# Kernel optimization log

Hardware: AMD Instinct MI355X
Metric: run time of the kernel (lower is better)

The kernel has to match this reference:

```python
import jax, jax.numpy as jnp
import numpy as np

N_LAYERS = 2
H = 16                      # num_heads
ARW = (1.0, 1.0)            # att_residual_weight
MCB = (0.0, 1.0)            # mask_clip_balancer
LN_EPS = 1e-5


def _ln(x, g, b):
    mu = jnp.mean(x, axis=-1, keepdims=True)
    var = jnp.mean(jnp.square(x - mu), axis=-1, keepdims=True)
    return (x - mu) * jax.lax.rsqrt(var + LN_EPS) * g + b


def _quick_gelu(u):
    return u * jax.nn.sigmoid(1.702 * u)


def setup_inputs() -> dict:
    key = jax.random.key(0)
    ks = jax.random.split(key, 8)
    L, B, C = 577, 8, 1024
    d_ff = 4 * C
    inp = {
        'x': jax.random.normal(ks[0], (L, B, C), jnp.float32),
        'att_bias': jax.random.normal(ks[1], (N_LAYERS, B * H, L, L), jnp.float32),
        'ln1_g': jnp.ones((N_LAYERS, C), jnp.float32),
        'ln1_b': jnp.zeros((N_LAYERS, C), jnp.float32),
        'in_w': 0.02 * jax.random.normal(ks[2], (N_LAYERS, 3 * C, C), jnp.float32),
        'in_b': jnp.zeros((N_LAYERS, 3 * C), jnp.float32),
        'out_w': 0.02 * jax.random.normal(ks[3], (N_LAYERS, C, C), jnp.float32),
        'out_b': jnp.zeros((N_LAYERS, C), jnp.float32),
        'ln2_g': jnp.ones((N_LAYERS, C), jnp.float32),
        'ln2_b': jnp.zeros((N_LAYERS, C), jnp.float32),
        'fc1_w': 0.02 * jax.random.normal(ks[4], (N_LAYERS, d_ff, C), jnp.float32),
        'fc1_b': jnp.zeros((N_LAYERS, d_ff), jnp.float32),
        'fc2_w': 0.02 * jax.random.normal(ks[5], (N_LAYERS, C, d_ff), jnp.float32),
        'fc2_b': jnp.zeros((N_LAYERS, C), jnp.float32),
    }
    return inp


def reference(x, att_bias, ln1_g, ln1_b, in_w, in_b, out_w, out_b,
              ln2_g, ln2_b, fc1_w, fc1_b, fc2_w, fc2_b):
    L, B, C = x.shape
    d = C // H
    scale = d ** -0.5  # custom_att_factor is None
    for i in range(N_LAYERS):
        # --- custom CSA attention ---
        h = _ln(x, ln1_g[i], ln1_b[i])                              # [L,B,C]
        qkv = jnp.einsum('lbc,fc->lbf', h, in_w[i]) + in_b[i]       # [L,B,3C]
        q, k, v = jnp.split(qkv, 3, axis=-1)
        to_heads = lambda t: t.reshape(L, B, H, d).transpose(1, 2, 0, 3)  # [B,H,L,d]
        q, k, v = to_heads(q), to_heads(k), to_heads(v)
        bias = att_bias[i].reshape(B, H, L, L)
        q_attn = bias + scale * jnp.einsum('bhld,bhmd->bhlm', q, q)
        k_attn = bias + scale * jnp.einsum('bhld,bhmd->bhlm', k, k)
        attn = jax.nn.softmax(q_attn, axis=-1) + jax.nn.softmax(k_attn, axis=-1)
        attn = attn * 0.5                                           # norm_att=True
        attn = jnp.mean(attn, axis=1, keepdims=True)                # avg_att=True -> [B,1,L,L]
        out = jnp.matmul(attn, v)                                   # broadcast over H -> [B,H,L,d]
        out = MCB[0] * v + MCB[1] * out
        out = out.transpose(2, 0, 1, 3).reshape(L, B, C)
        out = jnp.einsum('lbc,oc->lbo', out, out_w[i]) + out_b[i]
        x = ARW[0] * x + ARW[1] * out
        # --- MLP residual ---
        h2 = _ln(x, ln2_g[i], ln2_b[i])
        u = _quick_gelu(jnp.einsum('lbc,fc->lbf', h2, fc1_w[i]) + fc1_b[i])
        x = x + jnp.einsum('lbf,cf->lbc', u, fc2_w[i]) + fc2_b[i]
    return x
```

## Files before the change

kernel.cpp:

```cpp
#include <hip/hip_runtime.h>

typedef float f32x4 __attribute__((ext_vector_type(4)));
typedef __bf16 bf16x8 __attribute__((ext_vector_type(8)));

#define L_SEQ 577
#define BB 8
#define CC 1024
#define HH 16
#define ROWS (L_SEQ*BB)

static __device__ __forceinline__ ushort f2b(float f) {
  unsigned u = __float_as_uint(f);
  u += 0x7fffu + ((u >> 16) & 1u);
  return (ushort)(u >> 16);
}

static __device__ __forceinline__ void gld16(const void* g, void* l) {
  __builtin_amdgcn_global_load_lds((const __attribute__((address_space(1))) void*)g,
                                   (__attribute__((address_space(3))) void*)l, 16, 0, 0);
}

__global__ void cvt4_kernel(const float* __restrict__ s0, ushort* __restrict__ d0, int n0,
                            const float* __restrict__ s1, ushort* __restrict__ d1, int n1,
                            const float* __restrict__ s2, ushort* __restrict__ d2, int n2,
                            const float* __restrict__ s3, ushort* __restrict__ d3, int n3)
{
  int i = blockIdx.x * blockDim.x + threadIdx.x;
  const float* src; ushort* dst;
  if (i < n0)                { src = s0; dst = d0; }
  else if ((i -= n0) < n1)   { src = s1; dst = d1; }
  else if ((i -= n1) < n2)   { src = s2; dst = d2; }
  else if ((i -= n2) < n3)   { src = s3; dst = d3; }
  else return;
  float4 v = *(const float4*)(src + (size_t)i * 4);
  ushort4 o;
  o.x = f2b(v.x); o.y = f2b(v.y); o.z = f2b(v.z); o.w = f2b(v.w);
  *(ushort4*)(dst + (size_t)i * 4) = o;
}

template<int NP, bool DOLN>
__global__ __launch_bounds__(256)
void ln_resid_kernel(const float* __restrict__ xsrc, const float* __restrict__ parts,
                     const float* __restrict__ cbias,
                     const float* __restrict__ g, const float* __restrict__ be,
                     float* __restrict__ xdst, ushort* __restrict__ hout)
{
  const int row = blockIdx.x;
  const int t = threadIdx.x;
  float4 v = *(const float4*)(xsrc + (size_t)row * CC + t * 4);
  if (NP > 0) {
    float4 c4 = *(const float4*)(cbias + t * 4);
    v.x += c4.x; v.y += c4.y; v.z += c4.z; v.w += c4.w;
    #pragma unroll
    for (int p = 0; p < NP; ++p) {
      float4 pv = *(const float4*)(parts + ((size_t)p * ROWS + row) * CC + t * 4);
      v.x += pv.x; v.y += pv.y; v.z += pv.z; v.w += pv.w;
    }
  }
  *(float4*)(xdst + (size_t)row * CC + t * 4) = v;
  if (DOLN) {
    float s  = v.x + v.y + v.z + v.w;
    float s2 = v.x*v.x + v.y*v.y + v.z*v.z + v.w*v.w;
    #pragma unroll
    for (int sd = 1; sd < 64; sd <<= 1) { s += __shfl_xor(s, sd, 64); s2 += __shfl_xor(s2, sd, 64); }
    __shared__ float ps[4], ps2[4];
    const int w = t >> 6;
    if ((t & 63) == 0) { ps[w] = s; ps2[w] = s2; }
    __syncthreads();
    s  = ps[0] + ps[1] + ps[2] + ps[3];
    s2 = ps2[0] + ps2[1] + ps2[2] + ps2[3];
    const float mean = s * (1.f / 1024.f);
    const float var  = s2 * (1.f / 1024.f) - mean * mean;
    const float rstd = rsqrtf(var + 1e-5f);
    float4 gv = *(const float4*)(g + t * 4);
    float4 bv = *(const float4*)(be + t * 4);
    ushort4 o;
    o.x = f2b((v.x - mean) * rstd * gv.x + bv.x);
    o.y = f2b((v.y - mean) * rstd * gv.y + bv.y);
    o.z = f2b((v.z - mean) * rstd * gv.z + bv.z);
    o.w = f2b((v.w - mean) * rstd * gv.w + bv.w);
    *(ushort4*)(hout + (size_t)row * CC + t * 4) = o;
  }
}

__global__ __launch_bounds__(256)
void vt_kernel(const ushort* __restrict__ qkv, ushort* __restrict__ vt)
{
  __shared__ ushort tile[32][33];
  const int lt = blockIdx.x * 32;
  const int nt = blockIdx.y * 32;
  const int b  = blockIdx.z;
  const int tx = threadIdx.x & 31;
  const int ty = threadIdx.x >> 5;
  #pragma unroll
  for (int p = 0; p < 4; ++p) {
    int l = lt + ty + p * 8;
    ushort v = 0;
    if (l < L_SEQ) v = qkv[((size_t)l * BB + b) * 3072 + 2048 + nt + tx];
    tile[ty + p * 8][tx] = v;
  }
  __syncthreads();
  #pragma unroll
  for (int p = 0; p < 4; ++p) {
    int n = nt + ty + p * 8;
    int l = lt + tx;
    vt[((size_t)b * 1024 + n) * 608 + l] = tile[tx][ty + p * 8];
  }
}

__global__ __launch_bounds__(512, 3)
void attn_kernel(const ushort* __restrict__ qkv,
                 const float* __restrict__ bias,
                 ushort* __restrict__ attnp)
{
  __shared__ float2 red[2][8][16];
  const int t = threadIdx.x;
  const int lane = t & 63;
  const int w = t >> 6;
  const int fr = lane & 15;
  const int lq = lane >> 4;
  const int rb = blockIdx.x;
  const int b  = blockIdx.y;
  const int hg = blockIdx.z;
  const int r0 = rb * 16;
  const int rowl = min(r0 + fr, L_SEQ - 1);
  const size_t rbase = ((size_t)rowl * BB + b) * 3072;
  const int kc = lq * 8;

  float acc[5][4];
  #pragma unroll
  for (int it = 0; it < 5; ++it)
    #pragma unroll
    for (int r = 0; r < 4; ++r) acc[it][r] = 0.f;

  for (int h4 = 0; h4 < 4; ++h4) {
    const int h = hg * 4 + h4;
    const float* brow = bias + (((size_t)(b * HH + h)) * L_SEQ + rowl) * L_SEQ;
    #pragma unroll
    for (int v = 0; v < 2; ++v) {
      const int off = (v ? CC : 0) + h * 64;
      const bf16x8 rf0 = *(const bf16x8*)(qkv + rbase + off + kc);
      const bf16x8 rf1 = *(const bf16x8*)(qkv + rbase + off + 32 + kc);
      float s[5][4];
      #pragma unroll
      for (int it = 0; it < 5; ++it) {
        const int nt = w + it * 8;
        if (nt < 37) {
          const int crow = min(nt * 16 + fr, L_SEQ - 1);
          const size_t cb = ((size_t)crow * BB + b) * 3072;
          const bf16x8 cf0 = *(const bf16x8*)(qkv + cb + off + kc);
          const bf16x8 cf1 = *(const bf16x8*)(qkv + cb + off + 32 + kc);
          f32x4 d = {0.f, 0.f, 0.f, 0.f};
          d = __builtin_amdgcn_mfma_f32_16x16x32_bf16(cf0, rf0, d, 0, 0, 0);
          d = __builtin_amdgcn_mfma_f32_16x16x32_bf16(cf1, rf1, d, 0, 0, 0);
          const int c0 = nt * 16 + lq * 4;
          #pragma unroll
          for (int r = 0; r < 4; ++r)
            s[it][r] = (c0 + r < L_SEQ) ? (brow[c0 + r] + 0.125f * d[r]) : -1e30f;
        } else {
          #pragma unroll
          for (int r = 0; r < 4; ++r) s[it][r] = -1e30f;
        }
      }
      float mw = -1e30f;
      #pragma unroll
      for (int it = 0; it < 5; ++it)
        #pragma unroll
        for (int r = 0; r < 4; ++r) mw = fmaxf(mw, s[it][r]);
      mw = fmaxf(mw, __shfl_xor(mw, 16, 64));
      mw = fmaxf(mw, __shfl_xor(mw, 32, 64));
      float sw = 0.f;
      #pragma unroll
      for (int it = 0; it < 5; ++it)
        #pragma unroll
        for (int r = 0; r < 4; ++r) { s[it][r] = __expf(s[it][r] - mw); sw += s[it][r]; }
      sw += __shfl_xor(sw, 16, 64);
      sw += __shfl_xor(sw, 32, 64);
      if (lane < 16) red[v][w][lane] = make_float2(mw, sw);
      __syncthreads();
      float m = -1e30f;
      #pragma unroll
      for (int ww = 0; ww < 8; ++ww) m = fmaxf(m, red[v][ww][fr].x);
      float sm = 0.f;
      #pragma unroll
      for (int ww = 0; ww < 8; ++ww) {
        const float2 p = red[v][ww][fr];
        sm += p.y * __expf(p.x - m);
      }
      const float f = 0.03125f * __expf(mw - m) / sm;
      #pragma unroll
      for (int it = 0; it < 5; ++it)
        #pragma unroll
        for (int r = 0; r < 4; ++r) acc[it][r] += s[it][r] * f;
    }
  }
  if (r0 + fr < L_SEQ) {
    ushort* dst = attnp + ((size_t)hg * 8 + b) * 608 * 608 + (size_t)(r0 + fr) * 608;
    #pragma unroll
    for (int it = 0; it < 5; ++it) {
      const int nt = w + it * 8;
      if (nt < 37) {
        ushort4 o;
        o.x = f2b(acc[it][0]); o.y = f2b(acc[it][1]);
        o.z = f2b(acc[it][2]); o.w = f2b(acc[it][3]);
        *(ushort4*)(dst + nt * 16 + lq * 4) = o;
      }
    }
  }
}

__global__ __launch_bounds__(256)
void attn_combine(const ushort* __restrict__ attnp, ushort* __restrict__ attn)
{
  const int t = threadIdx.x;
  if (t >= 152) return;
  const int l = blockIdx.x;
  const int b = blockIdx.y;
  const int c0 = t * 4;
  const size_t base = ((size_t)b * 608 + l) * 608 + c0;
  const size_t hs = (size_t)8 * 608 * 608;
  float s[4] = {0.f, 0.f, 0.f, 0.f};
  #pragma unroll
  for (int p = 0; p < 4; ++p) {
    ushort4 v = *(const ushort4*)(attnp + p * hs + base);
    s[0] += __uint_as_float((unsigned)v.x << 16);
    s[1] += __uint_as_float((unsigned)v.y << 16);
    s[2] += __uint_as_float((unsigned)v.z << 16);
    s[3] += __uint_as_float((unsigned)v.w << 16);
  }
  ushort4 o;
  const bool lv = (l < L_SEQ);
  o.x = (lv && c0 + 0 < L_SEQ) ? f2b(s[0]) : (ushort)0;
  o.y = (lv && c0 + 1 < L_SEQ) ? f2b(s[1]) : (ushort)0;
  o.z = (lv && c0 + 2 < L_SEQ) ? f2b(s[2]) : (ushort)0;
  o.w = (lv && c0 + 3 < L_SEQ) ? f2b(s[3]) : (ushort)0;
  *(ushort4*)(attn + base) = o;
}

__global__ __launch_bounds__(256, 2)
void av_gemm(const ushort* __restrict__ A, int lda, int Arows, long aStride,
             const ushort* __restrict__ B, int ldb, long bStride,
             int M, int K,
             ushort* __restrict__ outb, int ldo)
{
  __shared__ __align__(16) ushort As[128 * 32];
  __shared__ __align__(16) ushort Bs[128 * 32];
  const int t = threadIdx.x;
  const int lane = t & 63;
  const int w = t >> 6;
  const int bm = blockIdx.x, bn = blockIdx.y, bz = blockIdx.z;
  const ushort* Ab = A + (long)bz * aStride;
  const ushort* Bb = B + (long)bz * bStride;
  const int srow = t >> 2;
  const int sc = (t & 3) * 8;
  const int wr = (w >> 1) * 64;
  const int wc = (w & 1) * 64;
  const int am1 = Arows - 1;
  f32x4 acc[4][4] = {};

  const int r0a = bm * 128 + srow;
  const int r0b = bn * 128 + srow;
  for (int kt = 0; kt < K; kt += 32) {
    __syncthreads();
    gld16(Ab + (size_t)min(r0a, am1) * lda + kt + sc, (void*)(As + t * 8));
    gld16(Ab + (size_t)min(r0a + 64, am1) * lda + kt + sc, (void*)(As + 2048 + t * 8));
    gld16(Bb + (size_t)r0b * ldb + kt + sc, (void*)(Bs + t * 8));
    gld16(Bb + (size_t)(r0b + 64) * ldb + kt + sc, (void*)(Bs + 2048 + t * 8));
    asm volatile("s_waitcnt vmcnt(0)" ::: "memory");
    __syncthreads();
    bf16x8 av[4], bv[4];
    const int fr = lane & 15;
    const int kc = (lane >> 4) * 8;
    #pragma unroll
    for (int m = 0; m < 4; ++m) av[m] = *(const bf16x8*)(As + (wr + m * 16 + fr) * 32 + kc);
    #pragma unroll
    for (int n = 0; n < 4; ++n) bv[n] = *(const bf16x8*)(Bs + (wc + n * 16 + fr) * 32 + kc);
    #pragma unroll
    for (int m = 0; m < 4; ++m)
      #pragma unroll
      for (int n = 0; n < 4; ++n)
        acc[m][n] = __builtin_amdgcn_mfma_f32_16x16x32_bf16(av[m], bv[n], acc[m][n], 0, 0, 0);
  }
  const int rbase = wr + (lane >> 4) * 4;
  const int cbase = wc + (lane & 15);
  #pragma unroll
  for (int n = 0; n < 4; ++n) {
    const int gn = bn * 128 + cbase + n * 16;
    #pragma unroll
    for (int m = 0; m < 4; ++m) {
      f32x4 d = acc[m][n];
      #pragma unroll
      for (int r = 0; r < 4; ++r) {
        const int gm = bm * 128 + rbase + m * 16 + r;
        if (gm < M) outb[((size_t)gm * 8 + bz) * ldo + gn] = f2b(d[r]);
      }
    }
  }
}

#define RD_A8(BOFS, MH) \
  _Pragma("unroll") for (int ks = 0; ks < 2; ++ks) \
  _Pragma("unroll") for (int m = 0; m < 4; ++m) \
    Af[ks][m] = rdA(BOFS, MH, ks, m);

#define RD_B4(BOFS, NH) \
  _Pragma("unroll") for (int ks = 0; ks < 2; ++ks) \
  _Pragma("unroll") for (int n = 0; n < 2; ++n) \
    Bf[NH][ks][n] = rdB(BOFS, NH, ks, n);

#define MFQ(MH, NH) \
  _Pragma("unroll") for (int ks = 0; ks < 2; ++ks) \
  _Pragma("unroll") for (int m = 0; m < 4; ++m) \
  _Pragma("unroll") for (int n = 0; n < 2; ++n) \
    acc[(MH)*4+m][(NH)*2+n] = __builtin_amdgcn_mfma_f32_16x16x32_bf16( \
        Af[ks][m], Bf[NH][ks][n], acc[(MH)*4+m][(NH)*2+n], 0, 0, 0);

#define BARO() \
  __builtin_amdgcn_sched_barrier(0); \
  __builtin_amdgcn_s_barrier(); \
  asm volatile("s_waitcnt lgkmcnt(0)" ::: "memory"); \
  __builtin_amdgcn_sched_barrier(0); \
  __builtin_amdgcn_s_setprio(1);

#define MF_END() \
  __builtin_amdgcn_s_setprio(0); \
  __builtin_amdgcn_sched_barrier(0); \
  __builtin_amdgcn_s_barrier();

template<int EPI>
__global__ __launch_bounds__(512, 2)
void gemm8(const ushort* __restrict__ Ap, int lda, int Arows,
           const ushort* __restrict__ Bp, int ldb,
           int M, int Ksplit,
           const float* __restrict__ bias,
           ushort* __restrict__ outb, float* __restrict__ outf, int ldo)
{
  __shared__ __align__(16) char smem[131072];
  const int t = threadIdx.x;
  const int lane = t & 63;
  const int w = t >> 6;
  const int wm = w >> 2, wn = w & 3;
  const int gx = gridDim.x;
  const int nwg = gx * gridDim.y;
  int id = blockIdx.y * gx + blockIdx.x;
  {
    const int q8 = nwg >> 3, r8 = nwg & 7;
    const int xcd = id & 7, pos = id >> 3;
    id = (xcd < r8 ? xcd * (q8 + 1) : r8 * (q8 + 1) + (xcd - r8) * q8) + pos;
  }
  const int bm = id % gx, bn = id / gx;
  const int bz = blockIdx.z;
  const int k0 = bz * Ksplit;
  const int iters = Ksplit >> 7;
  const int fr = lane & 15, lq = lane >> 4;

  f32x4 acc[8][4] = {};
  bf16x8 Af[2][4];
  bf16x8 Bf[2][2][2];

  const int rowj0 = t >> 3,        cbj0 = t & 7;
  const int rowj1 = (t + 512) >> 3, cbj1 = (t + 512) & 7;
  const ushort* pA[2][2]; const ushort* pB[2][2];
  #pragma unroll
  for (int h = 0; h < 2; ++h) {
    pA[h][0] = Ap + (size_t)min(bm*256 + h*128 + rowj0, Arows-1) * lda + k0 + ((cbj0 ^ (rowj0 & 7)) << 3);
    pA[h][1] = Ap + (size_t)min(bm*256 + h*128 + rowj1, Arows-1) * lda + k0 + ((cbj1 ^ (rowj1 & 7)) << 3);
    pB[h][0] = Bp + (size_t)(bn*256 + h*128 + rowj0) * ldb + k0 + ((cbj0 ^ (rowj0 & 7)) << 3);
    pB[h][1] = Bp + (size_t)(bn*256 + h*128 + rowj1) * ldb + k0 + ((cbj1 ^ (rowj1 & 7)) << 3);
  }

  auto stA = [&](int kt, int bofs, int h) {
    gld16(pA[h][0] + kt * 64, smem + bofs + h * 16384 + t * 16);
    gld16(pA[h][1] + kt * 64, smem + bofs + h * 16384 + (t + 512) * 16);
  };
  auto stB = [&](int kt, int bofs, int h) {
    gld16(pB[h][0] + kt * 64, smem + bofs + 32768 + h * 16384 + t * 16);
    gld16(pB[h][1] + kt * 64, smem + bofs + 32768 + h * 16384 + (t + 512) * 16);
  };
  auto rdA = [&](int bofs, int mh, int ks, int m) -> bf16x8 {
    const int rl = wm * 64 + m * 16 + fr;
    const int cb = (ks * 4 + lq) ^ (fr & 7);
    return *(const bf16x8*)(smem + bofs + mh * 16384 + rl * 128 + cb * 16);
  };
  auto rdB = [&](int bofs, int nh, int ks, int n) -> bf16x8 {
    const int rl = wn * 32 + n * 16 + fr;
    const int cb = (ks * 4 + lq) ^ (fr & 7);
    return *(const bf16x8*)(smem + bofs + 32768 + nh * 16384 + rl * 128 + cb * 16);
  };

  stA(0, 0, 0); stB(0, 0, 0); stB(0, 0, 1); stA(0, 0, 1);
  stA(1, 65536, 0); stB(1, 65536, 1); stA(1, 65536, 1);
  asm volatile("s_waitcnt vmcnt(6)" ::: "memory");
  __builtin_amdgcn_sched_barrier(0);
  __builtin_amdgcn_s_barrier();

  for (int i = 0; i < iters; ++i) {
    const bool more = (i + 1 < iters);
    const int kt2 = 2 * i + 2;
    RD_A8(0, 0) RD_B4(0, 0)
    stB(2 * i + 1, 65536, 0);
    BARO(); MFQ(0, 0) MF_END();
    RD_B4(0, 1)
    if (more) stA(kt2, 0, 0);
    BARO(); MFQ(0, 1) MF_END();
    RD_A8(0, 1)
    if (more) stB(kt2, 0, 1);
    BARO(); MFQ(1, 1) MF_END();
    if (more) stA(kt2, 0, 1);
    BARO(); MFQ(1, 0)
    __builtin_amdgcn_s_setprio(0);
    if (more) { asm volatile("s_waitcnt vmcnt(6)" ::: "memory"); }
    else      { asm volatile("s_waitcnt vmcnt(0)" ::: "memory"); }
    __builtin_amdgcn_sched_barrier(0);
    __builtin_amdgcn_s_barrier();
    RD_A8(65536, 0) RD_B4(65536, 0)
    if (more) stB(kt2, 0, 0);
    BARO(); MFQ(0, 0) MF_END();
    RD_B4(65536, 1)
    if (more) stA(2 * i + 3, 65536, 0);
    BARO(); MFQ(0, 1) MF_END();
    RD_A8(65536, 1)
    if (more) stB(2 * i + 3, 65536, 1);
    BARO(); MFQ(1, 1) MF_END();
    if (more) stA(2 * i + 3, 65536, 1);
    BARO(); MFQ(1, 0)
    __builtin_amdgcn_s_setprio(0);
    if (more) { asm volatile("s_waitcnt vmcnt(6)" ::: "memory"); }
    __builtin_amdgcn_sched_barrier(0);
    __builtin_amdgcn_s_barrier();
  }

  #pragma unroll
  for (int mh = 0; mh < 2; ++mh)
  #pragma unroll
  for (int nh = 0; nh < 2; ++nh)
  #pragma unroll
  for (int n = 0; n < 2; ++n) {
    const int gn = bn * 256 + nh * 128 + wn * 32 + n * 16 + fr;
    const float bval = (EPI == 4) ? 0.f : bias[gn];
    #pragma unroll
    for (int m = 0; m < 4; ++m) {
      f32x4 d = acc[mh * 4 + m][nh * 2 + n];
      #pragma unroll
      for (int r = 0; r < 4; ++r) {
        const int gm = bm * 256 + mh * 128 + wm * 64 + m * 16 + lq * 4 + r;
        if (gm < M) {
          if (EPI == 0) {
            outb[(size_t)gm * ldo + gn] = f2b(d[r] + bval);
          } else if (EPI == 1) {
            float v0 = d[r] + bval;
            outb[(size_t)gm * ldo + gn] = f2b(v0 / (1.f + __expf(-1.702f * v0)));
          } else {
            outf[((size_t)bz * M + gm) * ldo + gn] = d[r];
          }
        }
      }
    }
  }
}

extern "C" void kernel_launch(void* const* d_in, const int* in_sizes, int n_in,
                              void* d_out, int out_size, void* d_ws, size_t ws_size,
                              hipStream_t stream)
{
  (void)in_sizes; (void)n_in; (void)out_size; (void)ws_size;
  const float* x_in  = (const float*)d_in[0];
  const float* attb  = (const float*)d_in[1];
  const float* ln1_g = (const float*)d_in[2];
  const float* ln1_b = (const float*)d_in[3];
  const float* in_w  = (const float*)d_in[4];
  const float* in_b  = (const float*)d_in[5];
  const float* out_w = (const float*)d_in[6];
  const float* out_b = (const float*)d_in[7];
  const float* ln2_g = (const float*)d_in[8];
  const float* ln2_b = (const float*)d_in[9];
  const float* fc1_w = (const float*)d_in[10];
  const float* fc1_b = (const float*)d_in[11];
  const float* fc2_w = (const float*)d_in[12];
  const float* fc2_b = (const float*)d_in[13];
  float* x = (float*)d_out;

  char* ws = (char*)d_ws;
  size_t off = 0;
  auto alloc = [&](size_t bytes) -> void* {
    void* p = ws + off; off += (bytes + 255) & ~(size_t)255; return p;
  };
  ushort* wIn   = (ushort*)alloc(2ull * 3072 * 1024 * 2);
  ushort* wOut  = (ushort*)alloc(2ull * 1024 * 1024 * 2);
  ushort* wF1   = (ushort*)alloc(2ull * 4096 * 1024 * 2);
  ushort* wF2   = (ushort*)alloc(2ull * 4096 * 1024 * 2);
  ushort* hbuf  = (ushort*)alloc((size_t)ROWS * 1024 * 2);
  ushort* qkv   = (ushort*)alloc((size_t)ROWS * 3072 * 2);
  ushort* vt    = (ushort*)alloc((size_t)8 * 1024 * 608 * 2);
  ushort* attn  = (ushort*)alloc((size_t)8 * 608 * 608 * 2);
  ushort* attnp = (ushort*)alloc((size_t)4 * 8 * 608 * 608 * 2);
  ushort* outlb = (ushort*)alloc((size_t)ROWS * 1024 * 2);
  float*  pbuf  = (float*)alloc((size_t)4 * ROWS * 1024 * 4);
  ushort* ubuf  = qkv;

  cvt4_kernel<<<(1572864 + 524288 + 2097152 + 2097152 + 255) / 256, 256, 0, stream>>>(
      in_w,  wIn,  1572864,
      out_w, wOut, 524288,
      fc1_w, wF1,  2097152,
      fc2_w, wF2,  2097152);
  ln_resid_kernel<0, true><<<ROWS, 256, 0, stream>>>(x_in, nullptr, nullptr,
      ln1_g, ln1_b, x, hbuf);

  for (int i = 0; i < 2; ++i) {
    gemm8<0><<<dim3(19, 12, 1), 512, 0, stream>>>(hbuf, 1024, ROWS,
        wIn + (size_t)i * 3072 * 1024, 1024,
        ROWS, 1024, in_b + i * 3072, qkv, nullptr, 3072);
    attn_kernel<<<dim3(37, 8, 4), 512, 0, stream>>>(qkv, attb + (size_t)i * 128 * 577 * 577, attnp);
    vt_kernel<<<dim3(19, 32, 8), 256, 0, stream>>>(qkv, vt);
    attn_combine<<<dim3(608, 8), 256, 0, stream>>>(attnp, attn);
    av_gemm<<<dim3(5, 8, 8), 256, 0, stream>>>(attn, 608, 577, (long)608 * 608,
        vt, 608, (long)1024 * 608, 577, 608, outlb, 1024);
    gemm8<4><<<dim3(19, 4, 2), 512, 0, stream>>>(outlb, 1024, ROWS,
        wOut + (size_t)i * 1024 * 1024, 1024,
        ROWS, 512, nullptr, nullptr, pbuf, 1024);
    ln_resid_kernel<2, true><<<ROWS, 256, 0, stream>>>(x, pbuf, out_b + i * 1024,
        ln2_g + i * 1024, ln2_b + i * 1024, x, hbuf);
    gemm8<1><<<dim3(19, 16, 1), 512, 0, stream>>>(hbuf, 1024, ROWS,
        wF1 + (size_t)i * 4096 * 1024, 1024,
        ROWS, 1024, fc1_b + i * 4096, ubuf, nullptr, 4096);
    gemm8<4><<<dim3(19, 4, 4), 512, 0, stream>>>(ubuf, 4096, ROWS,
        wF2 + (size_t)i * 4096 * 1024, 4096,
        ROWS, 1024, nullptr, nullptr, pbuf, 1024);
    if (i == 0) {
      ln_resid_kernel<4, true><<<ROWS, 256, 0, stream>>>(x, pbuf, fc2_b,
          ln1_g + 1024, ln1_b + 1024, x, hbuf);
    } else {
      ln_resid_kernel<4, false><<<ROWS, 256, 0, stream>>>(x, pbuf, fc2_b + 1024,
          nullptr, nullptr, x, nullptr);
    }
  }
}
```

Measured before the change: 1.126 ms.

## Fuse Q and K softmax passes in attention kernel to share bias loads

```diff
diff --git a/kernel.cpp b/kernel.cpp
--- a/kernel.cpp
+++ b/kernel.cpp
@@ -108,20 +108,22 @@
   }
 }
 
-__global__ __launch_bounds__(512, 3)
+__global__ __launch_bounds__(512, 4)
 void attn_kernel(const ushort* __restrict__ qkv,
                  const float* __restrict__ bias,
                  ushort* __restrict__ attnp)
 {
-  __shared__ float2 red[2][8][16];
+  __shared__ float2 red[2][2][8][16];
   const int t = threadIdx.x;
   const int lane = t & 63;
   const int w = t >> 6;
   const int fr = lane & 15;
   const int lq = lane >> 4;
-  const int rb = blockIdx.x;
-  const int b  = blockIdx.y;
-  const int hg = blockIdx.z;
+  const int id = blockIdx.x;
+  const int b  = id & 7;
+  const int rem = id >> 3;
+  const int rb = rem % 37;
+  const int hg = rem / 37;
   const int r0 = rb * 16;
   const int rowl = min(r0 + fr, L_SEQ - 1);
   const size_t rbase = ((size_t)rowl * BB + b) * 3072;
@@ -135,64 +137,88 @@
 
   for (int h4 = 0; h4 < 4; ++h4) {
     const int h = hg * 4 + h4;
+    const int qoff = h * 64;
+    const int koff = CC + h * 64;
+    const bf16x8 rfq0 = *(const bf16x8*)(qkv + rbase + qoff + kc);
+    const bf16x8 rfq1 = *(const bf16x8*)(qkv + rbase + qoff + 32 + kc);
+    const bf16x8 rfk0 = *(const bf16x8*)(qkv + rbase + koff + kc);
+    const bf16x8 rfk1 = *(const bf16x8*)(qkv + rbase + koff + 32 + kc);
     const float* brow = bias + (((size_t)(b * HH + h)) * L_SEQ + rowl) * L_SEQ;
-    #pragma unroll
-    for (int v = 0; v < 2; ++v) {
-      const int off = (v ? CC : 0) + h * 64;
-      const bf16x8 rf0 = *(const bf16x8*)(qkv + rbase + off + kc);
-      const bf16x8 rf1 = *(const bf16x8*)(qkv + rbase + off + 32 + kc);
-      float s[5][4];
+    float sq[5][4], sk[5][4];
+    #pragma unroll
+    for (int it = 0; it < 5; ++it) {
+      const int nt = w + it * 8;
+      if (nt < 37) {
+        const int crow = min(nt * 16 + fr, L_SEQ - 1);
+        const size_t cb = ((size_t)crow * BB + b) * 3072;
+        const bf16x8 bq0 = *(const bf16x8*)(qkv + cb + qoff + kc);
+        const bf16x8 bq1 = *(const bf16x8*)(qkv + cb + qoff + 32 + kc);
+        const bf16x8 bk0 = *(const bf16x8*)(qkv + cb + koff + kc);
+        const bf16x8 bk1 = *(const bf16x8*)(qkv + cb + koff + 32 + kc);
+        const int c0 = nt * 16 + lq * 4;
+        float bs[4];
+        #pragma unroll
+        for (int r = 0; r < 4; ++r) bs[r] = brow[min(c0 + r, L_SEQ - 1)];
+        f32x4 dq = {0.f, 0.f, 0.f, 0.f};
+        f32x4 dk = {0.f, 0.f, 0.f, 0.f};
+        dq = __builtin_amdgcn_mfma_f32_16x16x32_bf16(bq0, rfq0, dq, 0, 0, 0);
+        dq = __builtin_amdgcn_mfma_f32_16x16x32_bf16(bq1, rfq1, dq, 0, 0, 0);
+        dk = __builtin_amdgcn_mfma_f32_16x16x32_bf16(bk0, rfk0, dk, 0, 0, 0);
+        dk = __builtin_amdgcn_mfma_f32_16x16x32_bf16(bk1, rfk1, dk, 0, 0, 0);
+        #pragma unroll
+        for (int r = 0; r < 4; ++r) {
+          const bool cv = (c0 + r < L_SEQ);
+          sq[it][r] = cv ? (bs[r] + 0.125f * dq[r]) : -1e30f;
+          sk[it][r] = cv ? (bs[r] + 0.125f * dk[r]) : -1e30f;
+        }
+      } else {
+        #pragma unroll
+        for (int r = 0; r < 4; ++r) { sq[it][r] = -1e30f; sk[it][r] = -1e30f; }
+      }
+    }
+    float mwq = -1e30f, mwk = -1e30f;
+    #pragma unroll
+    for (int it = 0; it < 5; ++it)
       #pragma unroll
-      for (int it = 0; it < 5; ++it) {
-        const int nt = w + it * 8;
-        if (nt < 37) {
-          const int crow = min(nt * 16 + fr, L_SEQ - 1);
-          const size_t cb = ((size_t)crow * BB + b) * 3072;
-          const bf16x8 cf0 = *(const bf16x8*)(qkv + cb + off + kc);
-          const bf16x8 cf1 = *(const bf16x8*)(qkv + cb + off + 32 + kc);
-          f32x4 d = {0.f, 0.f, 0.f, 0.f};
-          d = __builtin_amdgcn_mfma_f32_16x16x32_bf16(cf0, rf0, d, 0, 0, 0);
-          d = __builtin_amdgcn_mfma_f32_16x16x32_bf16(cf1, rf1, d, 0, 0, 0);
-          const int c0 = nt * 16 + lq * 4;
-          #pragma unroll
-          for (int r = 0; r < 4; ++r)
-            s[it][r] = (c0 + r < L_SEQ) ? (brow[c0 + r] + 0.125f * d[r]) : -1e30f;
-        } else {
-          #pragma unroll
-          for (int r = 0; r < 4; ++r) s[it][r] = -1e30f;
-        }
+      for (int r = 0; r < 4; ++r) { mwq = fmaxf(mwq, sq[it][r]); mwk = fmaxf(mwk, sk[it][r]); }
+    mwq = fmaxf(mwq, __shfl_xor(mwq, 16, 64)); mwq = fmaxf(mwq, __shfl_xor(mwq, 32, 64));
+    mwk = fmaxf(mwk, __shfl_xor(mwk, 16, 64)); mwk = fmaxf(mwk, __shfl_xor(mwk, 32, 64));
+    float swq = 0.f, swk = 0.f;
+    #pragma unroll
+    for (int it = 0; it < 5; ++it)
+      #pragma unroll
+      for (int r = 0; r < 4; ++r) {
+        sq[it][r] = __expf(sq[it][r] - mwq); swq += sq[it][r];
+        sk[it][r] = __expf(sk[it][r] - mwk); swk += sk[it][r];
       }
-      float mw = -1e30f;
+    swq += __shfl_xor(swq, 16, 64); swq += __shfl_xor(swq, 32, 64);
+    swk += __shfl_xor(swk, 16, 64); swk += __shfl_xor(swk, 32, 64);
+    const int p = h4 & 1;
+    if (lane < 16) {
+      red[p][0][w][lane] = make_float2(mwq, swq);
+      red[p][1][w][lane] = make_float2(mwk, swk);
+    }
+    __syncthreads();
+    float mq = -1e30f, mk = -1e30f;
+    #pragma unroll
+    for (int ww = 0; ww < 8; ++ww) {
+      mq = fmaxf(mq, red[p][0][ww][fr].x);
+      mk = fmaxf(mk, red[p][1][ww][fr].x);
+    }
+    float smq = 0.f, smk = 0.f;
+    #pragma unroll
+    for (int ww = 0; ww < 8; ++ww) {
+      const float2 pq = red[p][0][ww][fr];
+      const float2 pk = red[p][1][ww][fr];
+      smq += pq.y * __expf(pq.x - mq);
+      smk += pk.y * __expf(pk.x - mk);
+    }
+    const float fq = 0.03125f * __expf(mwq - mq) / smq;
+    const float fk = 0.03125f * __expf(mwk - mk) / smk;
+    #pragma unroll
+    for (int it = 0; it < 5; ++it)
       #pragma unroll
-      for (int it = 0; it < 5; ++it)
-        #pragma unroll
-        for (int r = 0; r < 4; ++r) mw = fmaxf(mw, s[it][r]);
-      mw = fmaxf(mw, __shfl_xor(mw, 16, 64));
-      mw = fmaxf(mw, __shfl_xor(mw, 32, 64));
-      float sw = 0.f;
-      #pragma unroll
-      for (int it = 0; it < 5; ++it)
-        #pragma unroll
-        for (int r = 0; r < 4; ++r) { s[it][r] = __expf(s[it][r] - mw); sw += s[it][r]; }
-      sw += __shfl_xor(sw, 16, 64);
-      sw += __shfl_xor(sw, 32, 64);
-      if (lane < 16) red[v][w][lane] = make_float2(mw, sw);
-      __syncthreads();
-      float m = -1e30f;
-      #pragma unroll
-      for (int ww = 0; ww < 8; ++ww) m = fmaxf(m, red[v][ww][fr].x);
-      float sm = 0.f;
-      #pragma unroll
-      for (int ww = 0; ww < 8; ++ww) {
-        const float2 p = red[v][ww][fr];
-        sm += p.y * __expf(p.x - m);
-      }
-      const float f = 0.03125f * __expf(mw - m) / sm;
-      #pragma unroll
-      for (int it = 0; it < 5; ++it)
-        #pragma unroll
-        for (int r = 0; r < 4; ++r) acc[it][r] += s[it][r] * f;
-    }
+      for (int r = 0; r < 4; ++r) acc[it][r] += sq[it][r] * fq + sk[it][r] * fk;
   }
   if (r0 + fr < L_SEQ) {
     ushort* dst = attnp + ((size_t)hg * 8 + b) * 608 * 608 + (size_t)(r0 + fr) * 608;
@@ -510,7 +536,7 @@
     gemm8<0><<<dim3(19, 12, 1), 512, 0, stream>>>(hbuf, 1024, ROWS,
         wIn + (size_t)i * 3072 * 1024, 1024,
         ROWS, 1024, in_b + i * 3072, qkv, nullptr, 3072);
-    attn_kernel<<<dim3(37, 8, 4), 512, 0, stream>>>(qkv, attb + (size_t)i * 128 * 577 * 577, attnp);
+    attn_kernel<<<dim3(1184, 1, 1), 512, 0, stream>>>(qkv, attb + (size_t)i * 128 * 577 * 577, attnp);
     vt_kernel<<<dim3(19, 32, 8), 256, 0, stream>>>(qkv, vt);
     attn_combine<<<dim3(608, 8), 256, 0, stream>>>(attnp, attn);
     av_gemm<<<dim3(5, 8, 8), 256, 0, stream>>>(attn, 608, 577, (long)608 * 608,
```

After: 1.062 ms. 5.7% less time.
